# Performance work log

Hardware: AMD Instinct MI355X
Metric: run time of the kernel (lower is better)

Reference implementation:

```python
import jax, jax.numpy as jnp
import numpy as np

B, D, E, NF, FD, H = 8192, 1024, 6, 32, 32, 256
MINK, MAXK = 1, 4

def _lin(a, w, b):
    return a @ w.T + b

def setup_inputs():
    key = jax.random.key(0)
    it = iter(jax.random.split(key, 60))
    def nrm(shape, s=0.02):
        return jax.random.normal(next(it), shape, jnp.float32) * s
    z = lambda *s: jnp.zeros(s, jnp.float32)
    return dict(
        x=jax.random.normal(next(it), (B, D), jnp.float32),
        esp_patterns=nrm((E, D), 1.0),
        sim_w1=nrm((D // 2, D)), sim_b1=z(D // 2),
        sim_w2=nrm((E, D // 2)), sim_b2=z(E),
        rout_w1=nrm((D // 2, D + E)), rout_b1=z(D // 2),
        rout_w2=nrm((E, D // 2)), rout_b2=z(E),
        kpred_w1=nrm((16, 6)), kpred_b1=z(16),
        kpred_w2=nrm((1, 16)), kpred_b2=z(1),
        sp_v_w=nrm((D, D)), sp_v_b=z(D),
        sp_o_w=nrm((D, D)), sp_o_b=z(D),
        sp_q1_w=nrm((D, D)), sp_q1_b=z(D),
        sp_q2_w=nrm((D, D)), sp_q2_b=z(D),
        de_w1=nrm((H, D)), de_b1=z(H),
        de_w2=nrm((D, H)), de_b2=z(D),
        de_g_w=nrm((D, D)), de_g_b=z(D),
        cf_in_w=nrm((3 * FD, FD)), cf_in_b=z(3 * FD),
        cf_o_w=nrm((FD, FD)), cf_o_b=z(FD),
        cf_f_w=nrm((FD, FD)), cf_f_b=z(FD),
        hf_w1=nrm((H, D)), hf_b1=z(H),
        hf_w2=nrm((D, H)), hf_b2=z(D),
        tc_w=nrm((4, 1, 3), 0.2), tc_b=z(4),
        tf_w=nrm((1, 4), 0.2), tf_b=z(1),
        lt_w1=nrm((H, D)), lt_b1=z(H),
        lt_w2=nrm((D, H)), lt_b2=z(D),
        op_w=nrm((D, D)), op_b=z(D),
    )

def reference(x, esp_patterns, sim_w1, sim_b1, sim_w2, sim_b2, rout_w1, rout_b1, rout_w2, rout_b2,
              kpred_w1, kpred_b1, kpred_w2, kpred_b2, sp_v_w, sp_v_b, sp_o_w, sp_o_b,
              sp_q1_w, sp_q1_b, sp_q2_w, sp_q2_b, de_w1, de_b1, de_w2, de_b2, de_g_w, de_g_b,
              cf_in_w, cf_in_b, cf_o_w, cf_o_b, cf_f_w, cf_f_b, hf_w1, hf_b1, hf_w2, hf_b2,
              tc_w, tc_b, tf_w, tf_b, lt_w1, lt_b1, lt_w2, lt_b2, op_w, op_b):
    # ---- FeatureAnalyzer ----
    sparsity = (x == 0).astype(jnp.float32).mean(-1)
    var_u = jnp.var(x, axis=-1, ddof=1)            # torch default unbiased var
    magnitude = jnp.abs(x).max(-1)
    norm = jnp.linalg.norm(x, axis=-1)
    mean = x.mean(-1, keepdims=True)
    std = jnp.sqrt(var_u[:, None] + 1e-8)
    skew = (((x - mean) / std) ** 3).mean(-1)
    s_abs = -jnp.sort(-jnp.abs(x), axis=-1)        # descending
    top20 = int(0.2 * D)
    conc = s_abs[:, :top20].sum(-1) / (s_abs.sum(-1) + 1e-8)
    feats = jnp.stack([sparsity, var_u, magnitude, norm, skew, conc], -1)  # (B,6)
    # ---- IntelligentRouter ----
    spec = jax.nn.sigmoid(x @ esp_patterns.T + _lin(jax.nn.relu(_lin(x, sim_w1, sim_b1)), sim_w2, sim_b2))
    probs = jax.nn.softmax(_lin(jax.nn.relu(_lin(jnp.concatenate([x, spec], -1), rout_w1, rout_b1)), rout_w2, rout_b2), -1)
    k_ratio = jax.nn.sigmoid(_lin(jax.nn.relu(_lin(feats, kpred_w1, kpred_b1)), kpred_w2, kpred_b2))[:, 0]
    k_vals = MINK + (MAXK - MINK) * k_ratio
    k = jnp.clip(jnp.floor(jnp.median(k_vals)), MINK, MAXK).astype(jnp.int32)  # int(median) truncation
    tp, ti = jax.lax.top_k(probs, MAXK)
    gmask = jnp.arange(MAXK) < k
    gates = jax.nn.softmax(jnp.where(gmask, tp, -jnp.inf), -1)  # (B,MAXK)
    # ---- experts (eval mode: dropout = identity) ----
    # SparseQuadraticExpert: seq-len-1 MHA collapses to V->out projections
    att = _lin(_lin(x, sp_v_w, sp_v_b), sp_o_w, sp_o_b)
    e_sp = _lin(jax.nn.relu(_lin(att * x, sp_q1_w, sp_q1_b)), sp_q2_w, sp_q2_b)
    # DenseQuadraticExpert
    e_de = _lin(jax.nn.relu(_lin(x, de_w1, de_b1)), de_w2, de_b2) + jax.nn.sigmoid(_lin(x, de_g_w, de_g_b)) * x
    # CrossFieldQuadraticExpert: single-head attention over fields
    xf = x.reshape(-1, NF, FD)
    q, kk, v = jnp.split(_lin(xf, cf_in_w, cf_in_b), 3, axis=-1)
    attn = jax.nn.softmax(jnp.einsum('bqd,bkd->bqk', q, kk) / jnp.sqrt(jnp.float32(FD)), -1)
    att_f = _lin(jnp.einsum('bqk,bkd->bqd', attn, v), cf_o_w, cf_o_b)
    e_cf = _lin(att_f * xf, cf_f_w, cf_f_b).reshape(-1, D)
    # HighFreqQuadraticExpert
    filt = _lin(jnp.tanh(_lin(x, hf_w1, hf_b1)), hf_w2, hf_b2)
    e_hf = x + (filt - x) * x
    # TemporalQuadraticExpert (AdaptiveAvgPool1d(D) on length-D input == identity)
    conv = jax.nn.relu(jax.lax.conv_general_dilated(x[:, None, :], tc_w, (1,), [(1, 1)], dimension_numbers=('NCH', 'OIH', 'NCH')) + tc_b[None, :, None])
    wts = jax.nn.sigmoid(_lin(conv.transpose(0, 2, 1), tf_w, tf_b))[..., 0]  # (B,D)
    e_tp = (x * wts) * x
    # LongTailQuadraticExpert
    t = _lin(jax.nn.elu(_lin(x, lt_w1, lt_b1)), lt_w2, lt_b2)
    e_lt = jnp.sign(x) * jnp.sqrt(jnp.abs(t * x) + 1e-8)
    # ---- dispatch + combine ----
    stack = jnp.stack([e_sp, e_de, e_cf, e_hf, e_tp, e_lt], axis=1)  # (B,E,D)
    sel = jnp.take_along_axis(stack, ti[:, :, None], axis=1)         # (B,MAXK,D)
    comb = (gates[:, :, None] * sel).sum(1)
    return _lin(comb, op_w, op_b) + x  # output projection + residual; Identity norm (batch_norm=False)
```

## Files before the change

kernel.cpp:

```cpp
#include <hip/hip_runtime.h>
#include <stdint.h>

typedef unsigned short u16;
typedef __attribute__((ext_vector_type(2))) float f32x2;
typedef __attribute__((ext_vector_type(4))) float f32x4;
typedef __attribute__((ext_vector_type(4))) unsigned short u16x4;
typedef __attribute__((ext_vector_type(8))) short short8;

#define DEV static __device__ __forceinline__

DEV float bf2f(u16 u){ union{unsigned int i; float f;} v; v.i=((unsigned int)u)<<16; return v.f; }
DEV u16 f2bf(float f){ union{float f; unsigned int i;} v; v.f=f; unsigned int u=v.i;
  return (u16)((u + 0x7FFFu + ((u>>16)&1u))>>16); }
DEV float wred(float v){ for(int o=32;o;o>>=1) v += __shfl_xor(v,o); return v; }
DEV float wredmax(float v){ for(int o=32;o;o>>=1) v = fmaxf(v,__shfl_xor(v,o)); return v; }
DEV int wredi(int v){ for(int o=32;o;o>>=1) v += __shfl_xor(v,o); return v; }

DEV void gload16(const void* g, void* l){
  __builtin_amdgcn_global_load_lds((const __attribute__((address_space(1))) unsigned int*)g,
                                   (__attribute__((address_space(3))) unsigned int*)l, 16, 0, 0);
}

DEV float actf(int ACT, float v){
  if(ACT==1) return v>0.f?v:0.f;
  if(ACT==2) return 1.f/(1.f+__expf(-v));
  if(ACT==3) return tanhf(v);
  if(ACT==4) return v>0.f?v:(__expf(v)-1.f);
  return v;
}

__global__ void cvt_kernel(const float* __restrict__ s, u16* __restrict__ d, int n4){
  for(int i=blockIdx.x*blockDim.x+threadIdx.x; i<n4; i+=gridDim.x*blockDim.x){
    f32x4 v=((const f32x4*)s)[i];
    u16x4 o;
    #pragma unroll
    for(int j=0;j<4;++j) o[j]=f2bf(v[j]);
    ((u16x4*)d)[i]=o;
  }
}

__global__ void cvt6_kernel(
    const float* __restrict__ s0, const float* __restrict__ s1, const float* __restrict__ s2,
    const float* __restrict__ s3, const float* __restrict__ s4, const float* __restrict__ s5,
    u16* __restrict__ d0, u16* __restrict__ d1, u16* __restrict__ d2,
    u16* __restrict__ d3, u16* __restrict__ d4, u16* __restrict__ d5, int n4each){
  const float* ss[6]={s0,s1,s2,s3,s4,s5};
  u16* dd[6]={d0,d1,d2,d3,d4,d5};
  const int total=6*n4each;
  for(int i=blockIdx.x*blockDim.x+threadIdx.x; i<total; i+=gridDim.x*blockDim.x){
    int b=i/n4each, r=i-b*n4each;
    f32x4 v=((const f32x4*)ss[b])[r];
    u16x4 o;
    #pragma unroll
    for(int j=0;j<4;++j) o[j]=f2bf(v[j]);
    ((u16x4*)dd[b])[r]=o;
  }
}

__global__ void cvt_split(const float* __restrict__ s, u16* __restrict__ hi, u16* __restrict__ lo, int n4){
  for(int i=blockIdx.x*blockDim.x+threadIdx.x; i<n4; i+=gridDim.x*blockDim.x){
    f32x4 v=((const f32x4*)s)[i];
    u16x4 h,l;
    #pragma unroll
    for(int j=0;j<4;++j){ h[j]=f2bf(v[j]); l[j]=f2bf(v[j]-bf2f(h[j])); }
    ((u16x4*)hi)[i]=h; ((u16x4*)lo)[i]=l;
  }
}

__global__ void cvt_split_rw1(const float* __restrict__ src, u16* __restrict__ hi, u16* __restrict__ lo){
  for(int i=blockIdx.x*blockDim.x+threadIdx.x; i<512*1024; i+=gridDim.x*blockDim.x){
    int r=i>>10, c=i&1023;
    float v=src[(size_t)r*1030+c];
    u16 h=f2bf(v);
    hi[i]=h; lo[i]=f2bf(v-bf2f(h));
  }
}

__global__ __launch_bounds__(256) void transpose_bf(const float* __restrict__ src, u16* __restrict__ dst){
  __shared__ float t[32][33];
  const int bx=blockIdx.x&31, by=blockIdx.x>>5;
  const int lx=threadIdx.x&31, ly=threadIdx.x>>5;
  #pragma unroll
  for(int r=0;r<4;++r)
    t[ly+8*r][lx] = src[(size_t)(by*32+ly+8*r)*1024 + bx*32+lx];
  __syncthreads();
  #pragma unroll
  for(int r=0;r<4;++r)
    dst[(size_t)(bx*32+ly+8*r)*1024 + by*32+lx] = f2bf(t[lx][ly+8*r]);
}

__global__ __launch_bounds__(256) void bias_comp(const float* __restrict__ ow, const float* __restrict__ vb,
    const float* __restrict__ ob, float* __restrict__ bc){
  const int wv=threadIdx.x>>6, lane=threadIdx.x&63;
  const int rowi=blockIdx.x*4+wv;
  float s=0.f;
  const float* wr=ow+(size_t)rowi*1024;
  #pragma unroll
  for(int j=0;j<16;++j) s+=wr[j*64+lane]*vb[j*64+lane];
  s=wred(s);
  if(lane==0) bc[rowi]=ob[rowi]+s;
}

__global__ void pack_b768(const float* __restrict__ b0, const float* __restrict__ b1,
                          const float* __restrict__ b2, float* __restrict__ o){
  int i=blockIdx.x*blockDim.x+threadIdx.x;
  if(i<256) o[i]=b0[i];
  else if(i<512) o[i]=b1[i-256];
  else if(i<768) o[i]=b2[i-512];
}

template<int ACT, int EPI>
__global__ __launch_bounds__(256) void gemm_bt(
    const u16* __restrict__ A, const u16* __restrict__ W,
    const float* __restrict__ bias, const u16* __restrict__ auxb,
    const float* __restrict__ auxf, const float* __restrict__ wsel,
    float* __restrict__ comb, void* __restrict__ Cv, int M, int N, int K, int lda)
{
  __shared__ __align__(16) u16 lA[128*64];
  __shared__ __align__(16) u16 lB[128*64];
  const int tid=threadIdx.x, lane=tid&63, wv=tid>>6;
  const int wr=wv>>1, wc=wv&1;
  const int bn=blockIdx.x*128, bm=blockIdx.y*128;
  f32x4 acc[4][4];
  #pragma unroll
  for(int m=0;m<4;++m){
    #pragma unroll
    for(int n=0;n<4;++n) acc[m][n]=(f32x4)0.f;
  }
  const int srow = wv*8 + (lane>>3);
  const int scol = (lane&7)*8;
  for(int kt=0;kt<K;kt+=64){
    #pragma unroll
    for(int i=0;i<4;++i){
      gload16(A + (size_t)(bm + i*32 + srow)*lda + kt + scol, &lA[(i*32 + wv*8)*64]);
      gload16(W + (size_t)(bn + i*32 + srow)*K + kt + scol, &lB[(i*32 + wv*8)*64]);
    }
    __syncthreads();
    #pragma unroll
    for(int kk=0;kk<2;++kk){
      const int fr=lane&15, kc=kk*32+(lane>>4)*8;
      short8 af[4], bfr[4];
      #pragma unroll
      for(int m=0;m<4;++m) af[m]=*(const short8*)&lA[(wr*64+m*16+fr)*64+kc];
      #pragma unroll
      for(int n=0;n<4;++n) bfr[n]=*(const short8*)&lB[(wc*64+n*16+fr)*64+kc];
      #pragma unroll
      for(int m=0;m<4;++m){
        #pragma unroll
        for(int n=0;n<4;++n)
          acc[m][n]=__builtin_amdgcn_mfma_f32_16x16x32_bf16(af[m],bfr[n],acc[m][n],0,0,0);
      }
    }
    __syncthreads();
  }
  const int fr=lane&15, fq=lane>>4;
  #pragma unroll
  for(int m=0;m<4;++m){
    #pragma unroll
    for(int n=0;n<4;++n){
      const int col = bn + wc*64 + n*16 + fr;
      const float bv = bias ? bias[col] : 0.f;
      #pragma unroll
      for(int j=0;j<4;++j){
        const int row = bm + wr*64 + m*16 + fq*4 + j;
        const size_t idx = (size_t)row*N+col;
        float v = acc[m][n][j] + bv;
        if(ACT==5){
          v = (col<256) ? fmaxf(v,0.f) : (col<512 ? tanhf(v) : (v>0.f?v:(__expf(v)-1.f)));
        } else v = actf(ACT, v);
        if(EPI==0){ ((u16*)Cv)[idx]=f2bf(v); }
        else if(EPI==1){ ((float*)Cv)[idx]=v; }
        else if(EPI==2){ ((u16*)Cv)[idx]=f2bf(v*auxf[idx]); }
        else if(EPI==3){ comb[idx]=wsel[row*6+0]*v; }
        else if(EPI==4){ comb[idx]+=wsel[row*6+1]*(v + bf2f(auxb[idx])*auxf[idx]); }
        else if(EPI==5){ float x0=auxf[idx]; comb[idx]+=wsel[row*6+3]*(x0+(v-x0)*x0); }
        else if(EPI==6){
          float x0=auxf[idx];
          float sg=(x0>0.f)?1.f:((x0<0.f)?-1.f:0.f);
          comb[idx]+=wsel[row*6+5]*sg*sqrtf(fabsf(v*x0)+1e-8f);
        }
        else { ((float*)Cv)[idx]=v+auxf[idx]; }
      }
    }
  }
}

template<int ACT>
__global__ __launch_bounds__(256) void gemm_split(
    const u16* __restrict__ Ah, const u16* __restrict__ Al,
    const u16* __restrict__ Wh, const u16* __restrict__ Wl,
    const float* __restrict__ bias, float* __restrict__ C, int M, int N, int K)
{
  const int LDL=40;
  __shared__ __align__(16) u16 lAh[128*40], lAl[128*40], lBh[64*40], lBl[64*40];
  const int tid=threadIdx.x, lane=tid&63, wv=tid>>6;
  const int wr=wv>>1, wc=wv&1;
  const int bn=blockIdx.x*64, bm=blockIdx.y*128;
  f32x4 acc[4][2];
  #pragma unroll
  for(int m=0;m<4;++m){
    #pragma unroll
    for(int n=0;n<2;++n) acc[m][n]=(f32x4)0.f;
  }
  const int srow=tid>>2, scol=(tid&3)*8;
  for(int kt=0;kt<K;kt+=32){
    short8 rah[2],ral[2],rbh,rbl;
    #pragma unroll
    for(int i=0;i<2;++i){
      size_t ao=(size_t)(bm+i*64+srow)*K+kt+scol;
      rah[i]=*(const short8*)(Ah+ao); ral[i]=*(const short8*)(Al+ao);
    }
    {
      size_t bo=(size_t)(bn+srow)*K+kt+scol;
      rbh=*(const short8*)(Wh+bo); rbl=*(const short8*)(Wl+bo);
    }
    __syncthreads();
    #pragma unroll
    for(int i=0;i<2;++i){
      int d=(i*64+srow)*LDL+scol;
      *(short8*)&lAh[d]=rah[i]; *(short8*)&lAl[d]=ral[i];
    }
    {
      int d=srow*LDL+scol;
      *(short8*)&lBh[d]=rbh; *(short8*)&lBl[d]=rbl;
    }
    __syncthreads();
    const int fr=lane&15, kc=(lane>>4)*8;
    short8 ah[4],al[4],bh[2],bl[2];
    #pragma unroll
    for(int m=0;m<4;++m){ int r=(wr*64+m*16+fr)*LDL+kc; ah[m]=*(const short8*)&lAh[r]; al[m]=*(const short8*)&lAl[r]; }
    #pragma unroll
    for(int n=0;n<2;++n){ int r=(wc*32+n*16+fr)*LDL+kc; bh[n]=*(const short8*)&lBh[r]; bl[n]=*(const short8*)&lBl[r]; }
    #pragma unroll
    for(int m=0;m<4;++m){
      #pragma unroll
      for(int n=0;n<2;++n){
        acc[m][n]=__builtin_amdgcn_mfma_f32_16x16x32_bf16(ah[m],bh[n],acc[m][n],0,0,0);
        acc[m][n]=__builtin_amdgcn_mfma_f32_16x16x32_bf16(ah[m],bl[n],acc[m][n],0,0,0);
        acc[m][n]=__builtin_amdgcn_mfma_f32_16x16x32_bf16(al[m],bh[n],acc[m][n],0,0,0);
      }
    }
  }
  const int fr=lane&15, fq=lane>>4;
  #pragma unroll
  for(int m=0;m<4;++m){
    #pragma unroll
    for(int n=0;n<2;++n){
      const int col = bn + wc*32 + n*16 + fr;
      const float bv = bias[col];
      #pragma unroll
      for(int j=0;j<4;++j){
        const int row = bm + wr*64 + m*16 + fq*4 + j;
        C[(size_t)row*N+col] = actf(ACT, acc[m][n][j] + bv);
      }
    }
  }
}

__global__ __launch_bounds__(256) void feats_kernel(const float* __restrict__ x,
    const float* __restrict__ kw1, const float* __restrict__ kb1,
    const float* __restrict__ kw2, const float* __restrict__ kb2,
    float* __restrict__ kvals)
{
  const int lane=threadIdx.x&63, wv=threadIdx.x>>6;
  const int row=blockIdx.x*4+wv;
  const float* xr=x+(size_t)row*1024;
  float xv[16]; unsigned int cd[16];
  float s=0.f, ss=0.f, sa=0.f, nz=0.f, amax=0.f;
  #pragma unroll
  for(int t=0;t<4;++t){
    f32x4 v=((const f32x4*)xr)[t*64+lane];
    #pragma unroll
    for(int j=0;j<4;++j){
      float f=v[j];
      union{float f;unsigned int i;} c; c.f=f;
      xv[t*4+j]=f; cd[t*4+j]=c.i&0x7fffffffu;
      s+=f; ss+=f*f; float a=fabsf(f); sa+=a; amax=fmaxf(amax,a); if(f==0.f) nz+=1.f;
    }
  }
  s=wred(s); ss=wred(ss); sa=wred(sa); nz=wred(nz); amax=wredmax(amax);
  const float mean=s/1024.f;
  const float var=(ss - s*mean)/1023.f;
  const float inv=1.f/sqrtf(var+1e-8f);
  float sk=0.f;
  #pragma unroll
  for(int j=0;j<16;++j){ float z=(xv[j]-mean)*inv; sk+=z*z*z; }
  sk=wred(sk);
  unsigned int lo=0u, hi=0x7f800000u;
  while(hi-lo>1u){
    unsigned int mid=(lo+hi)>>1;
    int c=0;
    #pragma unroll
    for(int j=0;j<16;++j) c += (cd[j] >= mid);
    c=wredi(c);
    if(c>=204) lo=mid; else hi=mid;
  }
  const unsigned int T=lo;
  float sg=0.f, cg=0.f;
  #pragma unroll
  for(int j=0;j<16;++j){ if(cd[j] > T){ sg+=fabsf(xv[j]); cg+=1.f; } }
  sg=wred(sg); cg=wred(cg);
  if(lane==0){
    union{unsigned int i;float f;} tv; tv.i=T;
    float conc=(sg + (204.f-cg)*tv.f)/(sa + 1e-8f);
    float feats[6]={ nz/1024.f, var, amax, sqrtf(ss), sk/1024.f, conc };
    float out=kb2[0];
    #pragma unroll
    for(int i=0;i<16;++i){
      float hv=kb1[i];
      #pragma unroll
      for(int j=0;j<6;++j) hv+=kw1[i*6+j]*feats[j];
      hv=fmaxf(hv,0.f);
      out+=kw2[i]*hv;
    }
    kvals[row]=1.f + 3.f*(1.f/(1.f+__expf(-out)));
  }
}

__global__ __launch_bounds__(256) void median_kernel(const float* __restrict__ kvals, int* __restrict__ kint){
  __shared__ unsigned int v[8192];
  __shared__ int hist4[4*257];
  __shared__ unsigned int selT;
  __shared__ int selR;
  const int tid=threadIdx.x, lane=tid&63, wv=tid>>6;
  for(int i=tid;i<8192;i+=256){ union{float f;unsigned int u;} c; c.f=kvals[i]; v[i]=c.u; }
  __syncthreads();
  unsigned int res[2];
  for(int t=0;t<2;++t){
    int r = 8192 - (4096+t) + 1;
    unsigned int prefix=0u;
    for(int lvl=0;lvl<4;++lvl){
      const int shift=24-lvl*8;
      const unsigned int pmask = (lvl==0)?0u:(0xFFFFFFFFu<<(shift+8));
      for(int i=tid;i<4*257;i+=256) hist4[i]=0;
      __syncthreads();
      for(int i=tid;i<8192;i+=256){
        unsigned int c=v[i];
        if((c&pmask)==prefix) atomicAdd(&hist4[wv*257+((c>>shift)&0xFFu)],1);
      }
      __syncthreads();
      if(wv==0){
        int h[4]; int ls=0;
        #pragma unroll
        for(int b=0;b<4;++b){
          int bin=lane*4+b;
          h[b]=hist4[bin]+hist4[257+bin]+hist4[514+bin]+hist4[771+bin];
          ls+=h[b];
        }
        int pfx=ls;
        #pragma unroll
        for(int off=1;off<64;off<<=1){ int tt=__shfl_up(pfx,off); if(lane>=off) pfx+=tt; }
        int total=__shfl(pfx,63);
        int cgt = total - pfx;
        #pragma unroll
        for(int b=3;b>=0;--b){
          if(cgt < r && r <= cgt + h[b]){
            selT = prefix | ((unsigned int)(lane*4+b)<<shift);
            selR = r - cgt;
          }
          cgt += h[b];
        }
      }
      __syncthreads();
      prefix=selT; r=selR;
      __syncthreads();
    }
    res[t]=prefix;
  }
  if(tid==0){
    union{unsigned int u; float f;} a,b; a.u=res[0]; b.u=res[1];
    float med=0.5f*(a.f+b.f);
    int k=(int)floorf(med);
    k = k<1?1:(k>4?4:k);
    *kint=k;
  }
}

__global__ __launch_bounds__(256) void spec_kernel(const float* __restrict__ x, const float* __restrict__ h,
    const float* __restrict__ esp, const float* __restrict__ w2, const float* __restrict__ b2,
    float* __restrict__ spec){
  const int wv=threadIdx.x>>6, lane=threadIdx.x&63;
  const int row=blockIdx.x*4+wv;
  const float* xr=x+(size_t)row*1024;
  const float* hr=h+(size_t)row*512;
  float xv[16], hv[8];
  #pragma unroll
  for(int j=0;j<16;++j) xv[j]=xr[j*64+lane];
  #pragma unroll
  for(int j=0;j<8;++j) hv[j]=hr[j*64+lane];
  for(int e=0;e<6;++e){
    float s=0.f;
    #pragma unroll
    for(int j=0;j<16;++j) s+=xv[j]*esp[e*1024+j*64+lane];
    #pragma unroll
    for(int j=0;j<8;++j) s+=hv[j]*w2[e*512+j*64+lane];
    s=wred(s);
    if(lane==0) spec[row*6+e]=1.f/(1.f+__expf(-(s+b2[e])));
  }
}

__global__ void rout_fix(float* __restrict__ h, const float* __restrict__ spec, const float* __restrict__ rw1){
  const int total=8192*128;
  for(int i=blockIdx.x*blockDim.x+threadIdx.x;i<total;i+=gridDim.x*blockDim.x){
    int row=i>>7, j0=(i&127)*4;
    const float* sp=&spec[row*6];
    f32x4 hv=((f32x4*)h)[i];
    #pragma unroll
    for(int j=0;j<4;++j){
      float v=hv[j];
      int col=j0+j;
      #pragma unroll
      for(int e=0;e<6;++e) v+=sp[e]*rw1[(size_t)col*1030+1024+e];
      hv[j]=fmaxf(v,0.f);
    }
    ((f32x4*)h)[i]=hv;
  }
}

__global__ __launch_bounds__(256) void probs_kernel(const float* __restrict__ h, const float* __restrict__ w2,
    const float* __restrict__ b2, float* __restrict__ probs){
  const int wv=threadIdx.x>>6, lane=threadIdx.x&63;
  const int row=blockIdx.x*4+wv;
  const float* hr=h+(size_t)row*512;
  float hv[8];
  #pragma unroll
  for(int j=0;j<8;++j) hv[j]=hr[j*64+lane];
  float lg[6];
  #pragma unroll
  for(int e=0;e<6;++e){
    float s=0.f;
    #pragma unroll
    for(int j=0;j<8;++j) s+=hv[j]*w2[e*512+j*64+lane];
    lg[e]=wred(s)+b2[e];
  }
  if(lane==0){
    float m=lg[0];
    #pragma unroll
    for(int e=1;e<6;++e) m=fmaxf(m,lg[e]);
    float den=0.f, ex[6];
    #pragma unroll
    for(int e=0;e<6;++e){ ex[e]=__expf(lg[e]-m); den+=ex[e]; }
    #pragma unroll
    for(int e=0;e<6;++e) probs[row*6+e]=ex[e]/den;
  }
}

__global__ void gates_kernel(const float* __restrict__ probs, const int* __restrict__ kint,
                             float* __restrict__ wsel){
  const int r=blockIdx.x*blockDim.x+threadIdx.x;
  if(r>=8192) return;
  const int k=*kint;
  float p[6];
  #pragma unroll
  for(int e=0;e<6;++e) p[e]=probs[r*6+e];
  float w[6]={0,0,0,0,0,0};
  bool used[6]={false,false,false,false,false,false};
  int idx[4]; float val[4];
  #pragma unroll
  for(int j=0;j<4;++j){
    int bi=0; float bv=-1e30f;
    #pragma unroll
    for(int e=0;e<6;++e) if(!used[e] && p[e]>bv){ bv=p[e]; bi=e; }
    used[bi]=true; idx[j]=bi; val[j]=bv;
  }
  float m=val[0], den=0.f, g[4]={0,0,0,0};
  for(int j=0;j<k;++j){ g[j]=__expf(val[j]-m); den+=g[j]; }
  for(int j=0;j<k;++j) w[idx[j]]=g[j]/den;
  #pragma unroll
  for(int e=0;e<6;++e) wsel[r*6+e]=w[e];
}

__global__ __launch_bounds__(256) void cf_kernel(const float* __restrict__ x,
    const float* __restrict__ w_in, const float* __restrict__ b_in,
    const float* __restrict__ w_o, const float* __restrict__ b_o,
    const float* __restrict__ w_f, const float* __restrict__ b_f,
    const float* __restrict__ wsel, float* __restrict__ comb){
  __shared__ __align__(16) u16 smem[6400 + 4*6144];
  const int tid=threadIdx.x, wv=tid>>6, lane=tid&63;
  const int fr=lane&15, fq=lane>>4;
  for(int i=tid;i<5120;i+=256){
    float v=(i<3072)? w_in[i] : (i<4096? w_o[i-3072] : w_f[i-4096]);
    smem[(i>>5)*40 + (i&31)] = f2bf(v);
  }
  u16* wb   = smem + 6400 + wv*6144;
  float* xfl= (float*)wb;
  u16* bufA = wb + 2304;
  u16* bufB = bufA + 1280;
  u16* bufC = bufB + 1280;
  const int row = blockIdx.x*4 + wv;
  const float* xr = x + (size_t)row*1024;
  #pragma unroll
  for(int t=0;t<4;++t){
    f32x4 v = ((const f32x4*)xr)[t*64+lane];
    int e=(t*64+lane)*4;
    *(f32x4*)&xfl[(e>>5)*36 + (e&31)] = v;
  }
  __syncthreads();
  short8 xa[2];
  #pragma unroll
  for(int ft=0;ft<2;++ft){
    f32x4 a=*(const f32x4*)&xfl[(ft*16+fr)*36 + fq*8];
    f32x4 b=*(const f32x4*)&xfl[(ft*16+fr)*36 + fq*8 + 4];
    short8 s;
    s[0]=(short)f2bf(a[0]); s[1]=(short)f2bf(a[1]); s[2]=(short)f2bf(a[2]); s[3]=(short)f2bf(a[3]);
    s[4]=(short)f2bf(b[0]); s[5]=(short)f2bf(b[1]); s[6]=(short)f2bf(b[2]); s[7]=(short)f2bf(b[3]);
    xa[ft]=s;
  }
  f32x4 acc1[2][6];
  #pragma unroll
  for(int ct=0;ct<6;++ct){
    short8 wfrag=*(const short8*)&smem[(ct*16+fr)*40 + fq*8];
    #pragma unroll
    for(int ft=0;ft<2;++ft)
      acc1[ft][ct]=__builtin_amdgcn_mfma_f32_16x16x32_bf16(xa[ft],wfrag,(f32x4)0.f,0,0,0);
  }
  float bi[6];
  #pragma unroll
  for(int ct=0;ct<6;++ct) bi[ct]=b_in[ct*16+fr];
  #pragma unroll
  for(int ct=0;ct<6;++ct){
    #pragma unroll
    for(int ft=0;ft<2;++ft){
      #pragma unroll
      for(int j=0;j<4;++j){
        u16 h=f2bf(acc1[ft][ct][j]+bi[ct]);
        int rg=ft*16+fq*4+j, cg=ct*16+fr;
        if(cg<32)      bufA[rg*40+cg]=h;
        else if(cg<64) bufB[rg*40+(cg-32)]=h;
        else           bufC[(cg-64)*40+rg]=h;
      }
    }
  }
  __syncthreads();
  short8 qa0=*(const short8*)&bufA[fr*40+fq*8];
  short8 qa1=*(const short8*)&bufA[(16+fr)*40+fq*8];
  short8 kb0=*(const short8*)&bufB[fr*40+fq*8];
  short8 kb1=*(const short8*)&bufB[(16+fr)*40+fq*8];
  f32x4 aS[2][2];
  aS[0][0]=__builtin_amdgcn_mfma_f32_16x16x32_bf16(qa0,kb0,(f32x4)0.f,0,0,0);
  aS[0][1]=__builtin_amdgcn_mfma_f32_16x16x32_bf16(qa0,kb1,(f32x4)0.f,0,0,0);
  aS[1][0]=__builtin_amdgcn_mfma_f32_16x16x32_bf16(qa1,kb0,(f32x4)0.f,0,0,0);
  aS[1][1]=__builtin_amdgcn_mfma_f32_16x16x32_bf16(qa1,kb1,(f32x4)0.f,0,0,0);
  const float scale=0.17677669529663687f;
  #pragma unroll
  for(int rt=0;rt<2;++rt){
    #pragma unroll
    for(int j=0;j<4;++j){
      float e0=aS[rt][0][j]*scale, e1=aS[rt][1][j]*scale;
      float m=fmaxf(e0,e1);
      #pragma unroll
      for(int o=1;o<16;o<<=1) m=fmaxf(m,__shfl_xor(m,o));
      e0=__expf(e0-m); e1=__expf(e1-m);
      float den=e0+e1;
      #pragma unroll
      for(int o=1;o<16;o<<=1) den+=__shfl_xor(den,o);
      float inv=1.f/den;
      bufA[(rt*16+fq*4+j)*40 + fr]      = f2bf(e0*inv);
      bufA[(rt*16+fq*4+j)*40 + 16+fr]   = f2bf(e1*inv);
    }
  }
  __syncthreads();
  short8 pa0=*(const short8*)&bufA[fr*40+fq*8];
  short8 pa1=*(const short8*)&bufA[(16+fr)*40+fq*8];
  short8 vb0=*(const short8*)&bufC[fr*40+fq*8];
  short8 vb1=*(const short8*)&bufC[(16+fr)*40+fq*8];
  f32x4 aA[2][2];
  aA[0][0]=__builtin_amdgcn_mfma_f32_16x16x32_bf16(pa0,vb0,(f32x4)0.f,0,0,0);
  aA[0][1]=__builtin_amdgcn_mfma_f32_16x16x32_bf16(pa0,vb1,(f32x4)0.f,0,0,0);
  aA[1][0]=__builtin_amdgcn_mfma_f32_16x16x32_bf16(pa1,vb0,(f32x4)0.f,0,0,0);
  aA[1][1]=__builtin_amdgcn_mfma_f32_16x16x32_bf16(pa1,vb1,(f32x4)0.f,0,0,0);
  #pragma unroll
  for(int rt=0;rt<2;++rt)
    #pragma unroll
    for(int dt=0;dt<2;++dt)
      #pragma unroll
      for(int j=0;j<4;++j)
        bufB[(rt*16+fq*4+j)*40 + dt*16+fr]=f2bf(aA[rt][dt][j]);
  __syncthreads();
  short8 aa0=*(const short8*)&bufB[fr*40+fq*8];
  short8 aa1=*(const short8*)&bufB[(16+fr)*40+fq*8];
  short8 ob0=*(const short8*)&smem[(96+fr)*40+fq*8];
  short8 ob1=*(const short8*)&smem[(112+fr)*40+fq*8];
  f32x4 aF[2][2];
  aF[0][0]=__builtin_amdgcn_mfma_f32_16x16x32_bf16(aa0,ob0,(f32x4)0.f,0,0,0);
  aF[0][1]=__builtin_amdgcn_mfma_f32_16x16x32_bf16(aa0,ob1,(f32x4)0.f,0,0,0);
  aF[1][0]=__builtin_amdgcn_mfma_f32_16x16x32_bf16(aa1,ob0,(f32x4)0.f,0,0,0);
  aF[1][1]=__builtin_amdgcn_mfma_f32_16x16x32_bf16(aa1,ob1,(f32x4)0.f,0,0,0);
  float bo[2]={b_o[fr], b_o[16+fr]};
  #pragma unroll
  for(int rt=0;rt<2;++rt){
    #pragma unroll
    for(int dt=0;dt<2;++dt){
      #pragma unroll
      for(int j=0;j<4;++j){
        int fld=rt*16+fq*4+j, d=dt*16+fr;
        float attf=aF[rt][dt][j]+bo[dt];
        bufC[fld*40+d]=f2bf(attf*xfl[fld*36+d]);
      }
    }
  }
  __syncthreads();
  short8 pr0=*(const short8*)&bufC[fr*40+fq*8];
  short8 pr1=*(const short8*)&bufC[(16+fr)*40+fq*8];
  short8 fb0=*(const short8*)&smem[(128+fr)*40+fq*8];
  short8 fb1=*(const short8*)&smem[(144+fr)*40+fq*8];
  f32x4 aE[2][2];
  aE[0][0]=__builtin_amdgcn_mfma_f32_16x16x32_bf16(pr0,fb0,(f32x4)0.f,0,0,0);
  aE[0][1]=__builtin_amdgcn_mfma_f32_16x16x32_bf16(pr0,fb1,(f32x4)0.f,0,0,0);
  aE[1][0]=__builtin_amdgcn_mfma_f32_16x16x32_bf16(pr1,fb0,(f32x4)0.f,0,0,0);
  aE[1][1]=__builtin_amdgcn_mfma_f32_16x16x32_bf16(pr1,fb1,(f32x4)0.f,0,0,0);
  float bff[2]={b_f[fr], b_f[16+fr]};
  const float w2=wsel[row*6+2];
  float* cb=&comb[(size_t)row*1024];
  #pragma unroll
  for(int rt=0;rt<2;++rt){
    #pragma unroll
    for(int dt=0;dt<2;++dt){
      #pragma unroll
      for(int j=0;j<4;++j){
        int fld=rt*16+fq*4+j, d=dt*16+fr;
        cb[fld*32+d]+=w2*(aE[rt][dt][j]+bff[dt]);
      }
    }
  }
}

__global__ __launch_bounds__(256) void tp_kernel(const float* __restrict__ x,
    const float* __restrict__ wsel, const float* __restrict__ comb,
    const float* __restrict__ tcw, const float* __restrict__ tcb,
    const float* __restrict__ tfw, const float* __restrict__ tfb,
    u16* __restrict__ obf){
  __shared__ float xs[1026];
  const int row=blockIdx.x, tid=threadIdx.x;
  f32x4 u=((const f32x4*)(x+(size_t)row*1024))[tid];
  #pragma unroll
  for(int j=0;j<4;++j) xs[1+4*tid+j]=u[j];
  if(tid==0){ xs[0]=0.f; xs[1025]=0.f; }
  __syncthreads();
  const float w4=wsel[row*6+4];
  float tc[4][3], tb[4], tf[4];
  #pragma unroll
  for(int o=0;o<4;++o){
    #pragma unroll
    for(int kh=0;kh<3;++kh) tc[o][kh]=tcw[o*3+kh];
    tb[o]=tcb[o]; tf[o]=tfw[o];
  }
  const float tfb0=tfb[0];
  f32x4 cv=((const f32x4*)(comb+(size_t)row*1024))[tid];
  u16x4 ov;
  #pragma unroll
  for(int j=0;j<4;++j){
    const int d=4*tid+j;
    float pre=tfb0;
    #pragma unroll
    for(int o=0;o<4;++o){
      float c=tb[o]+tc[o][0]*xs[d]+tc[o][1]*xs[d+1]+tc[o][2]*xs[d+2];
      pre+=tf[o]*fmaxf(c,0.f);
    }
    float wt=1.f/(1.f+__expf(-pre));
    float xv=xs[1+d];
    ov[j]=f2bf(cv[j]+w4*xv*xv*wt);
  }
  ((u16x4*)(obf+(size_t)row*1024))[tid]=ov;
}

extern "C" void kernel_launch(void* const* d_in, const int* in_sizes, int n_in,
                              void* d_out, int out_size, void* d_ws, size_t ws_size,
                              hipStream_t stream)
{
  const float* x     =(const float*)d_in[0];
  const float* esp   =(const float*)d_in[1];
  const float* sim_w1=(const float*)d_in[2],  *sim_b1=(const float*)d_in[3];
  const float* sim_w2=(const float*)d_in[4],  *sim_b2=(const float*)d_in[5];
  const float* rout_w1=(const float*)d_in[6], *rout_b1=(const float*)d_in[7];
  const float* rout_w2=(const float*)d_in[8], *rout_b2=(const float*)d_in[9];
  const float* kw1=(const float*)d_in[10], *kb1=(const float*)d_in[11];
  const float* kw2=(const float*)d_in[12], *kb2=(const float*)d_in[13];
  const float* spv_w=(const float*)d_in[14], *spv_b=(const float*)d_in[15];
  const float* spo_w=(const float*)d_in[16], *spo_b=(const float*)d_in[17];
  const float* spq1_w=(const float*)d_in[18], *spq1_b=(const float*)d_in[19];
  const float* spq2_w=(const float*)d_in[20], *spq2_b=(const float*)d_in[21];
  const float* de_w1=(const float*)d_in[22], *de_b1=(const float*)d_in[23];
  const float* de_w2=(const float*)d_in[24], *de_b2=(const float*)d_in[25];
  const float* de_gw=(const float*)d_in[26], *de_gb=(const float*)d_in[27];
  const float* cf_inw=(const float*)d_in[28], *cf_inb=(const float*)d_in[29];
  const float* cf_ow=(const float*)d_in[30], *cf_ob=(const float*)d_in[31];
  const float* cf_fw=(const float*)d_in[32], *cf_fb=(const float*)d_in[33];
  const float* hf_w1=(const float*)d_in[34], *hf_b1=(const float*)d_in[35];
  const float* hf_w2=(const float*)d_in[36], *hf_b2=(const float*)d_in[37];
  const float* tc_w=(const float*)d_in[38], *tc_b=(const float*)d_in[39];
  const float* tf_w=(const float*)d_in[40], *tf_b=(const float*)d_in[41];
  const float* lt_w1=(const float*)d_in[42], *lt_b1=(const float*)d_in[43];
  const float* lt_w2=(const float*)d_in[44], *lt_b2=(const float*)d_in[45];
  const float* op_w=(const float*)d_in[46], *op_b=(const float*)d_in[47];
  float* out=(float*)d_out;
  (void)in_sizes; (void)n_in; (void)out_size; (void)ws_size;

  constexpr int NB=8192;
  const size_t BD=(size_t)NB*1024;
  char* base=(char*)d_ws; size_t off=0;
  auto carve=[&](size_t n)->void*{ void* q=base+off; off+=(n+255)&~(size_t)255; return q; };
  float* comb =(float*)carve(BD*4);
  u16*  bufA =(u16*)carve(BD*2);
  u16*  bufB =(u16*)carve(BD*2);
  u16*  x_hi =(u16*)carve(BD*2);
  u16*  x_lo =(u16*)carve(BD*2);
  float* h512a=(float*)carve((size_t)NB*512*4);
  float* h512b=(float*)carve((size_t)NB*512*4);
  u16*  h768 =(u16*)carve((size_t)NB*768*2);
  u16* sw1h=(u16*)carve((size_t)512*1024*2);
  u16* sw1l=(u16*)carve((size_t)512*1024*2);
  u16* rw1h=(u16*)carve((size_t)512*1024*2);
  u16* rw1l=(u16*)carve((size_t)512*1024*2);
  u16* spv_bf =(u16*)carve((size_t)1024*1024*2);
  u16* spo_bf =(u16*)carve((size_t)1024*1024*2);
  u16* spq1_bf=(u16*)carve((size_t)1024*1024*2);
  u16* spq2_bf=(u16*)carve((size_t)1024*1024*2);
  u16* w768_bf=(u16*)carve((size_t)768*1024*2);
  u16* dew2_bf=(u16*)carve((size_t)1024*256*2);
  u16* degw_bf=(u16*)carve((size_t)1024*1024*2);
  u16* hfw2_bf=(u16*)carve((size_t)1024*256*2);
  u16* ltw2_bf=(u16*)carve((size_t)1024*256*2);
  u16* opw_bf =(u16*)carve((size_t)1024*1024*2);
  u16* spvT_bf=(u16*)carve((size_t)1024*1024*2);
  float* bc   =(float*)carve((size_t)1024*4);
  float* b768 =(float*)carve((size_t)768*4);
  float* spec=(float*)carve((size_t)NB*6*4);
  float* probs=(float*)carve((size_t)NB*6*4);
  float* wsel=(float*)carve((size_t)NB*6*4);
  float* kvals=(float*)carve((size_t)NB*4);
  int*   kint=(int*)carve(256);

  const dim3 blk(256);
  const dim3 gEW(2048);
  auto cgrid=[&](int n4)->dim3{ int g=(n4+255)/256; return dim3(g>2048?2048:g); };

  cvt_split<<<cgrid(2097152),blk,0,stream>>>(x, x_hi, x_lo, 2097152);
  cvt_split<<<cgrid(131072),blk,0,stream>>>(sim_w1, sw1h, sw1l, 131072);
  cvt_split_rw1<<<cgrid(131072),blk,0,stream>>>(rout_w1, rw1h, rw1l);
  cvt6_kernel<<<cgrid(6*262144),blk,0,stream>>>(spv_w,spo_w,spq1_w,spq2_w,de_gw,op_w,
                                                spv_bf,spo_bf,spq1_bf,spq2_bf,degw_bf,opw_bf, 262144);
  cvt6_kernel<<<cgrid(6*65536),blk,0,stream>>>(de_w1,de_w2,hf_w1,hf_w2,lt_w1,lt_w2,
                                               w768_bf,dew2_bf,w768_bf+262144,hfw2_bf,w768_bf+524288,ltw2_bf, 65536);
  transpose_bf<<<dim3(1024),blk,0,stream>>>(spv_w, spvT_bf);
  bias_comp<<<dim3(256),blk,0,stream>>>(spo_w, spv_b, spo_b, bc);
  pack_b768<<<dim3(3),blk,0,stream>>>(de_b1, hf_b1, lt_b1, b768);

  feats_kernel<<<dim3(2048),blk,0,stream>>>(x, kw1,kb1,kw2,kb2, kvals);
  median_kernel<<<dim3(1),blk,0,stream>>>(kvals, kint);
  gemm_split<1><<<dim3(8,64),blk,0,stream>>>(x_hi,x_lo, sw1h,sw1l, sim_b1, h512a, NB,512,1024);
  spec_kernel<<<gEW,blk,0,stream>>>(x, h512a, esp, sim_w2, sim_b2, spec);
  gemm_split<0><<<dim3(8,64),blk,0,stream>>>(x_hi,x_lo, rw1h,rw1l, rout_b1, h512b, NB,512,1024);
  rout_fix<<<gEW,blk,0,stream>>>(h512b, spec, rout_w1);
  probs_kernel<<<gEW,blk,0,stream>>>(h512b, rout_w2, rout_b2, probs);
  gates_kernel<<<dim3(32),blk,0,stream>>>(probs, kint, wsel);

  gemm_bt<0,1><<<dim3(8,8),blk,0,stream>>>(spo_bf, spvT_bf, nullptr, nullptr, nullptr, nullptr, nullptr, h512b, 1024,1024,1024,1024);
  cvt_kernel<<<cgrid(262144),blk,0,stream>>>(h512b, spv_bf, 262144);

  gemm_bt<0,2><<<dim3(8,64),blk,0,stream>>>(x_hi, spv_bf, bc, nullptr, x, nullptr, nullptr, bufB, NB,1024,1024,1024);
  gemm_bt<1,0><<<dim3(8,64),blk,0,stream>>>(bufB, spq1_bf, spq1_b, nullptr, nullptr, nullptr, nullptr, bufA, NB,1024,1024,1024);
  gemm_bt<0,3><<<dim3(8,64),blk,0,stream>>>(bufA, spq2_bf, spq2_b, nullptr, nullptr, wsel, comb, nullptr, NB,1024,1024,1024);

  gemm_bt<5,0><<<dim3(6,64),blk,0,stream>>>(x_hi, w768_bf, b768, nullptr, nullptr, nullptr, nullptr, h768, NB,768,1024,1024);

  gemm_bt<2,0><<<dim3(8,64),blk,0,stream>>>(x_hi, degw_bf, de_gb, nullptr, nullptr, nullptr, nullptr, bufB, NB,1024,1024,1024);
  gemm_bt<0,4><<<dim3(8,64),blk,0,stream>>>(h768, dew2_bf, de_b2, bufB, x, wsel, comb, nullptr, NB,1024,256,768);

  cf_kernel<<<dim3(2048),blk,0,stream>>>(x, cf_inw, cf_inb, cf_ow, cf_ob, cf_fw, cf_fb, wsel, comb);

  gemm_bt<0,5><<<dim3(8,64),blk,0,stream>>>(h768+256, hfw2_bf, hf_b2, nullptr, x, wsel, comb, nullptr, NB,1024,256,768);

  gemm_bt<0,6><<<dim3(8,64),blk,0,stream>>>(h768+512, ltw2_bf, lt_b2, nullptr, x, wsel, comb, nullptr, NB,1024,256,768);

  tp_kernel<<<dim3(NB),blk,0,stream>>>(x, wsel, comb, tc_w, tc_b, tf_w, tf_b, bufB);

  gemm_bt<0,7><<<dim3(8,64),blk,0,stream>>>(bufB, opw_bf, op_b, nullptr, x, nullptr, nullptr, out, NB,1024,1024,1024);
}
```

Measured before the change: 635.0 us.

## Fuse similarity and routing first-layer split GEMMs into one 1024-wide GEMM

Concatenates sim_w1 and rout_w1 (hi/lo split) into a single 1024x1024 weight and runs one split-precision GEMM with 128x128 tiles that writes both hidden halves into one buffer. ReLU is applied only to the first 512 columns, and downstream kernels now index the second half with a 1024 stride. It also remaps block indices so neighbouring workgroups are grouped by row band, aiming for better L2 reuse of the x tiles. The point is to read x once instead of twice, cut a launch, and raise MFMA work per tile. In exchange the per-column branch in the epilogue adds a little work, and the kernel uses more LDS and registers per block.

```diff
diff --git a/kernel.cpp b/kernel.cpp
--- a/kernel.cpp
+++ b/kernel.cpp
@@ -107,6 +107,12 @@
   if(i<256) o[i]=b0[i];
   else if(i<512) o[i]=b1[i-256];
   else if(i<768) o[i]=b2[i-512];
+}
+
+__global__ void pack_b1024(const float* __restrict__ b0, const float* __restrict__ b1, float* __restrict__ o){
+  int i=blockIdx.x*blockDim.x+threadIdx.x;
+  if(i<512) o[i]=b0[i];
+  else if(i<1024) o[i]=b1[i-512];
 }
 
 template<int ACT, int EPI>
@@ -185,56 +191,53 @@
   }
 }
 
-template<int ACT>
-__global__ __launch_bounds__(256) void gemm_split(
+__global__ __launch_bounds__(256) void gemm_split2(
     const u16* __restrict__ Ah, const u16* __restrict__ Al,
     const u16* __restrict__ Wh, const u16* __restrict__ Wl,
     const float* __restrict__ bias, float* __restrict__ C, int M, int N, int K)
 {
   const int LDL=40;
-  __shared__ __align__(16) u16 lAh[128*40], lAl[128*40], lBh[64*40], lBl[64*40];
+  __shared__ __align__(16) u16 lAh[128*40], lAl[128*40], lBh[128*40], lBl[128*40];
   const int tid=threadIdx.x, lane=tid&63, wv=tid>>6;
   const int wr=wv>>1, wc=wv&1;
-  const int bn=blockIdx.x*64, bm=blockIdx.y*128;
-  f32x4 acc[4][2];
+  const int nwg=gridDim.x;
+  const int wg=(blockIdx.x%8)*(nwg/8)+blockIdx.x/8;
+  const int bx=wg&7, by=wg>>3;
+  const int bn=bx*128, bm=by*128;
+  f32x4 acc[4][4];
   #pragma unroll
   for(int m=0;m<4;++m){
     #pragma unroll
-    for(int n=0;n<2;++n) acc[m][n]=(f32x4)0.f;
+    for(int n=0;n<4;++n) acc[m][n]=(f32x4)0.f;
   }
   const int srow=tid>>2, scol=(tid&3)*8;
   for(int kt=0;kt<K;kt+=32){
-    short8 rah[2],ral[2],rbh,rbl;
+    short8 rah[2],ral[2],rbh[2],rbl[2];
     #pragma unroll
     for(int i=0;i<2;++i){
       size_t ao=(size_t)(bm+i*64+srow)*K+kt+scol;
+      size_t bo=(size_t)(bn+i*64+srow)*K+kt+scol;
       rah[i]=*(const short8*)(Ah+ao); ral[i]=*(const short8*)(Al+ao);
-    }
-    {
-      size_t bo=(size_t)(bn+srow)*K+kt+scol;
-      rbh=*(const short8*)(Wh+bo); rbl=*(const short8*)(Wl+bo);
+      rbh[i]=*(const short8*)(Wh+bo); rbl[i]=*(const short8*)(Wl+bo);
     }
     __syncthreads();
     #pragma unroll
     for(int i=0;i<2;++i){
       int d=(i*64+srow)*LDL+scol;
       *(short8*)&lAh[d]=rah[i]; *(short8*)&lAl[d]=ral[i];
-    }
-    {
-      int d=srow*LDL+scol;
-      *(short8*)&lBh[d]=rbh; *(short8*)&lBl[d]=rbl;
+      *(short8*)&lBh[d]=rbh[i]; *(short8*)&lBl[d]=rbl[i];
     }
     __syncthreads();
     const int fr=lane&15, kc=(lane>>4)*8;
-    short8 ah[4],al[4],bh[2],bl[2];
+    short8 ah[4],al[4],bh[4],bl[4];
     #pragma unroll
     for(int m=0;m<4;++m){ int r=(wr*64+m*16+fr)*LDL+kc; ah[m]=*(const short8*)&lAh[r]; al[m]=*(const short8*)&lAl[r]; }
     #pragma unroll
-    for(int n=0;n<2;++n){ int r=(wc*32+n*16+fr)*LDL+kc; bh[n]=*(const short8*)&lBh[r]; bl[n]=*(const short8*)&lBl[r]; }
+    for(int n=0;n<4;++n){ int r=(wc*64+n*16+fr)*LDL+kc; bh[n]=*(const short8*)&lBh[r]; bl[n]=*(const short8*)&lBl[r]; }
     #pragma unroll
     for(int m=0;m<4;++m){
       #pragma unroll
-      for(int n=0;n<2;++n){
+      for(int n=0;n<4;++n){
         acc[m][n]=__builtin_amdgcn_mfma_f32_16x16x32_bf16(ah[m],bh[n],acc[m][n],0,0,0);
         acc[m][n]=__builtin_amdgcn_mfma_f32_16x16x32_bf16(ah[m],bl[n],acc[m][n],0,0,0);
         acc[m][n]=__builtin_amdgcn_mfma_f32_16x16x32_bf16(al[m],bh[n],acc[m][n],0,0,0);
@@ -245,13 +248,15 @@
   #pragma unroll
   for(int m=0;m<4;++m){
     #pragma unroll
-    for(int n=0;n<2;++n){
-      const int col = bn + wc*32 + n*16 + fr;
+    for(int n=0;n<4;++n){
+      const int col = bn + wc*64 + n*16 + fr;
       const float bv = bias[col];
       #pragma unroll
       for(int j=0;j<4;++j){
         const int row = bm + wr*64 + m*16 + fq*4 + j;
-        C[(size_t)row*N+col] = actf(ACT, acc[m][n][j] + bv);
+        float v = acc[m][n][j] + bv;
+        if(col<512) v=fmaxf(v,0.f);
+        C[(size_t)row*N+col] = v;
       }
     }
   }
@@ -382,7 +387,7 @@
   const int wv=threadIdx.x>>6, lane=threadIdx.x&63;
   const int row=blockIdx.x*4+wv;
   const float* xr=x+(size_t)row*1024;
-  const float* hr=h+(size_t)row*512;
+  const float* hr=h+(size_t)row*1024;
   float xv[16], hv[8];
   #pragma unroll
   for(int j=0;j<16;++j) xv[j]=xr[j*64+lane];
@@ -404,7 +409,7 @@
   for(int i=blockIdx.x*blockDim.x+threadIdx.x;i<total;i+=gridDim.x*blockDim.x){
     int row=i>>7, j0=(i&127)*4;
     const float* sp=&spec[row*6];
-    f32x4 hv=((f32x4*)h)[i];
+    f32x4 hv=*(f32x4*)&h[(size_t)row*1024+512+j0];
     #pragma unroll
     for(int j=0;j<4;++j){
       float v=hv[j];
@@ -413,7 +418,7 @@
       for(int e=0;e<6;++e) v+=sp[e]*rw1[(size_t)col*1030+1024+e];
       hv[j]=fmaxf(v,0.f);
     }
-    ((f32x4*)h)[i]=hv;
+    *(f32x4*)&h[(size_t)row*1024+512+j0]=hv;
   }
 }
 
@@ -421,7 +426,7 @@
     const float* __restrict__ b2, float* __restrict__ probs){
   const int wv=threadIdx.x>>6, lane=threadIdx.x&63;
   const int row=blockIdx.x*4+wv;
-  const float* hr=h+(size_t)row*512;
+  const float* hr=h+(size_t)row*1024+512;
   float hv[8];
   #pragma unroll
   for(int j=0;j<8;++j) hv[j]=hr[j*64+lane];
@@ -705,13 +710,10 @@
   u16*  bufB =(u16*)carve(BD*2);
   u16*  x_hi =(u16*)carve(BD*2);
   u16*  x_lo =(u16*)carve(BD*2);
-  float* h512a=(float*)carve((size_t)NB*512*4);
-  float* h512b=(float*)carve((size_t)NB*512*4);
+  float* h1024=(float*)carve(BD*4);
   u16*  h768 =(u16*)carve((size_t)NB*768*2);
-  u16* sw1h=(u16*)carve((size_t)512*1024*2);
-  u16* sw1l=(u16*)carve((size_t)512*1024*2);
-  u16* rw1h=(u16*)carve((size_t)512*1024*2);
-  u16* rw1l=(u16*)carve((size_t)512*1024*2);
+  u16* w1024h=(u16*)carve((size_t)1024*1024*2);
+  u16* w1024l=(u16*)carve((size_t)1024*1024*2);
   u16* spv_bf =(u16*)carve((size_t)1024*1024*2);
   u16* spo_bf =(u16*)carve((size_t)1024*1024*2);
   u16* spq1_bf=(u16*)carve((size_t)1024*1024*2);
@@ -725,6 +727,7 @@
   u16* spvT_bf=(u16*)carve((size_t)1024*1024*2);
   float* bc   =(float*)carve((size_t)1024*4);
   float* b768 =(float*)carve((size_t)768*4);
+  float* b1024=(float*)carve((size_t)1024*4);
   float* spec=(float*)carve((size_t)NB*6*4);
   float* probs=(float*)carve((size_t)NB*6*4);
   float* wsel=(float*)carve((size_t)NB*6*4);
@@ -736,8 +739,8 @@
   auto cgrid=[&](int n4)->dim3{ int g=(n4+255)/256; return dim3(g>2048?2048:g); };
 
   cvt_split<<<cgrid(2097152),blk,0,stream>>>(x, x_hi, x_lo, 2097152);
-  cvt_split<<<cgrid(131072),blk,0,stream>>>(sim_w1, sw1h, sw1l, 131072);
-  cvt_split_rw1<<<cgrid(131072),blk,0,stream>>>(rout_w1, rw1h, rw1l);
+  cvt_split<<<cgrid(131072),blk,0,stream>>>(sim_w1, w1024h, w1024l, 131072);
+  cvt_split_rw1<<<cgrid(131072),blk,0,stream>>>(rout_w1, w1024h+524288, w1024l+524288);
   cvt6_kernel<<<cgrid(6*262144),blk,0,stream>>>(spv_w,spo_w,spq1_w,spq2_w,de_gw,op_w,
                                                 spv_bf,spo_bf,spq1_bf,spq2_bf,degw_bf,opw_bf, 262144);
   cvt6_kernel<<<cgrid(6*65536),blk,0,stream>>>(de_w1,de_w2,hf_w1,hf_w2,lt_w1,lt_w2,
@@ -745,18 +748,18 @@
   transpose_bf<<<dim3(1024),blk,0,stream>>>(spv_w, spvT_bf);
   bias_comp<<<dim3(256),blk,0,stream>>>(spo_w, spv_b, spo_b, bc);
   pack_b768<<<dim3(3),blk,0,stream>>>(de_b1, hf_b1, lt_b1, b768);
+  pack_b1024<<<dim3(4),blk,0,stream>>>(sim_b1, rout_b1, b1024);
 
   feats_kernel<<<dim3(2048),blk,0,stream>>>(x, kw1,kb1,kw2,kb2, kvals);
   median_kernel<<<dim3(1),blk,0,stream>>>(kvals, kint);
-  gemm_split<1><<<dim3(8,64),blk,0,stream>>>(x_hi,x_lo, sw1h,sw1l, sim_b1, h512a, NB,512,1024);
-  spec_kernel<<<gEW,blk,0,stream>>>(x, h512a, esp, sim_w2, sim_b2, spec);
-  gemm_split<0><<<dim3(8,64),blk,0,stream>>>(x_hi,x_lo, rw1h,rw1l, rout_b1, h512b, NB,512,1024);
-  rout_fix<<<gEW,blk,0,stream>>>(h512b, spec, rout_w1);
-  probs_kernel<<<gEW,blk,0,stream>>>(h512b, rout_w2, rout_b2, probs);
+  gemm_split2<<<dim3(512),blk,0,stream>>>(x_hi,x_lo, w1024h,w1024l, b1024, h1024, NB,1024,1024);
+  spec_kernel<<<gEW,blk,0,stream>>>(x, h1024, esp, sim_w2, sim_b2, spec);
+  rout_fix<<<gEW,blk,0,stream>>>(h1024, spec, rout_w1);
+  probs_kernel<<<gEW,blk,0,stream>>>(h1024, rout_w2, rout_b2, probs);
   gates_kernel<<<dim3(32),blk,0,stream>>>(probs, kint, wsel);
 
-  gemm_bt<0,1><<<dim3(8,8),blk,0,stream>>>(spo_bf, spvT_bf, nullptr, nullptr, nullptr, nullptr, nullptr, h512b, 1024,1024,1024,1024);
-  cvt_kernel<<<cgrid(262144),blk,0,stream>>>(h512b, spv_bf, 262144);
+  gemm_bt<0,1><<<dim3(8,8),blk,0,stream>>>(spo_bf, spvT_bf, nullptr, nullptr, nullptr, nullptr, nullptr, h1024, 1024,1024,1024,1024);
+  cvt_kernel<<<cgrid(262144),blk,0,stream>>>(h1024, spv_bf, 262144);
 
   gemm_bt<0,2><<<dim3(8,64),blk,0,stream>>>(x_hi, spv_bf, bc, nullptr, x, nullptr, nullptr, bufB, NB,1024,1024,1024);
   gemm_bt<1,0><<<dim3(8,64),blk,0,stream>>>(bufB, spq1_bf, spq1_b, nullptr, nullptr, nullptr, nullptr, bufA, NB,1024,1024,1024);
```

After: 604.8 us. 4.7% less time.
